# Kernel tuning notes

Measured on AMD Instinct MI355X. Metric: run time of the kernel, lower is better.

Reference implementation:

```python
import jax, jax.numpy as jnp
import numpy as np

N_NODES = 32767   # complete binary tree, depth 15
EMB_DIM = 256
HIDDEN = 256      # 'hidden_size' -> LSTM state is 2*HIDDEN
VOCAB = 32        # len(ExprNode.TYPE_LIST)


def setup_inputs() -> dict:
    key = jax.random.key(0)
    k1, k2, k3, k4, k5, k6 = jax.random.split(key, 6)
    H2 = 2 * HIDDEN
    types = jax.random.randint(k1, (N_NODES,), 0, VOCAB, dtype=jnp.int32)
    # complete binary tree: children of node i are 2i+1 / 2i+2; sentinel slot N = zero state
    idx = np.arange(N_NODES)
    a = 2 * idx + 1
    b = 2 * idx + 2
    a = np.where(a < N_NODES, a, N_NODES).astype(np.int32)
    b = np.where(b < N_NODES, b, N_NODES).astype(np.int32)
    scale = 1.0 / np.sqrt(H2)
    return {
        "types": types,
        "a_idx": jnp.asarray(a),
        "b_idx": jnp.asarray(b),
        "emb": jax.random.normal(k2, (VOCAB, EMB_DIM), jnp.float32) * 0.02,
        "W_ih": jax.random.normal(k3, (4 * H2, EMB_DIM), jnp.float32) * scale,
        "W_hh": jax.random.normal(k4, (4 * H2, H2), jnp.float32) * scale,
        "b_ih": jax.random.normal(k5, (4 * H2,), jnp.float32) * scale,
        "b_hh": jax.random.normal(k6, (4 * H2,), jnp.float32) * scale,
    }


def reference(types, a_idx, b_idx, emb, W_ih, W_hh, b_ih, b_hh):
    """Recursive binary tree-LSTM over topological (leaves-first) order.
    Each node's LSTM state has size 2H; a parent's incoming (h, c) is the concat
    of the first H entries of each child's state (zeros for missing children).
    Returns per-node hidden outputs [N, 2H] (the out_map, indexed by node id)."""
    N = types.shape[0]
    H2 = W_hh.shape[1]
    H = H2 // 2
    # batched input projection for all nodes at once: [N, 4*H2]
    x_proj = emb[types] @ W_ih.T + (b_ih + b_hh)
    Hs0 = jnp.zeros((N + 1, H2), x_proj.dtype)  # slot N = h0 (zeros)
    Cs0 = jnp.zeros((N + 1, H2), x_proj.dtype)
    order = jnp.arange(N - 1, -1, -1)  # children (higher index) before parents

    def step(carry, i):
        Hs, Cs = carry
        h = jnp.concatenate([Hs[a_idx[i], :H], Hs[b_idx[i], :H]])  # [2H]
        c = jnp.concatenate([Cs[a_idx[i], :H], Cs[b_idx[i], :H]])
        gates = x_proj[i] + W_hh @ h                 # [4*H2], torch gate order i,f,g,o
        ig, fg, gg, og = jnp.split(gates, 4)
        c_new = jax.nn.sigmoid(fg) * c + jax.nn.sigmoid(ig) * jnp.tanh(gg)
        h_new = jax.nn.sigmoid(og) * jnp.tanh(c_new)
        return (Hs.at[i].set(h_new), Cs.at[i].set(c_new)), h_new

    _, outs = jax.lax.scan(step, (Hs0, Cs0), order)
    return outs[::-1]  # reorder so row i is node i's output
```

## Files before the change

### kernel.cpp

```cpp
#include <hip/hip_runtime.h>
#include <hip/hip_bf16.h>


#define NNODES 32767

typedef __attribute__((ext_vector_type(8))) short bf16x8;
typedef __attribute__((ext_vector_type(4))) float f32x4;

__device__ __forceinline__ float sigf(float x) { return 1.0f / (1.0f + __expf(-x)); }
__device__ __forceinline__ float tanhfast(float x) { return 2.0f / (1.0f + __expf(-2.0f * x)) - 1.0f; }

__device__ __forceinline__ short bf_hi(float x) {
    __hip_bfloat16 h = __float2bfloat16(x);
    return __builtin_bit_cast(short, h);
}
__device__ __forceinline__ float bf_f(short s) {
    __hip_bfloat16 h = __builtin_bit_cast(__hip_bfloat16, s);
    return __bfloat162float(h);
}
__device__ __forceinline__ void split8(const float* src, short* hi, short* lo) {
#pragma unroll
    for (int j = 0; j < 8; ++j) {
        float x = src[j];
        short h = bf_hi(x);
        hi[j] = h;
        lo[j] = bf_hi(x - bf_f(h));
    }
}

__global__ void proj_kernel(const float* __restrict__ emb, const float* __restrict__ W_ih,
                            const float* __restrict__ b_ih, const float* __restrict__ b_hh,
                            float* __restrict__ proj) {
    __shared__ float e[256];
    int v = blockIdx.x >> 3;
    int rc = blockIdx.x & 7;
    int t = threadIdx.x;
    e[t] = emb[v * 256 + t];
    __syncthreads();
    int r = rc * 256 + t;
    const float4* w4 = (const float4*)(W_ih + (size_t)r * 256);
    const float4* e4 = (const float4*)e;
    float acc = 0.f;
#pragma unroll 8
    for (int k = 0; k < 64; ++k) {
        float4 w = w4[k];
        float4 h = e4[k];
        acc += w.x * h.x + w.y * h.y + w.z * h.z + w.w * h.w;
    }
    proj[v * 2048 + r] = acc + b_ih[r] + b_hh[r];
}

__global__ void wpack_kernel(const float* __restrict__ W_hh,
                             short* __restrict__ Whi, short* __restrict__ Wlo) {
    int t = blockIdx.x * 256 + threadIdx.x;
    int lane = t & 63;
    int kt = (t >> 6) & 15;
    int ntile = t >> 10;
    int n = ntile * 16 + (lane & 15);
    int k0 = kt * 32 + (lane >> 4) * 8;
    const float* src = W_hh + (size_t)n * 512 + k0;
    short hi[8], lo[8];
    split8(src, hi, lo);
    *(bf16x8*)(Whi + (size_t)t * 8) = *(bf16x8*)hi;
    *(bf16x8*)(Wlo + (size_t)t * 8) = *(bf16x8*)lo;
}

__global__ void leaf_kernel(const int* __restrict__ types, const float* __restrict__ proj,
                            float* __restrict__ out, float* __restrict__ C256,
                            short* __restrict__ Hsplit) {
    int bi = blockIdx.x;
    int node = 16383 + (bi >> 1);
    int j = ((bi & 1) << 8) + threadIdx.x;
    int tt = types[node];
    const float* p = proj + (size_t)tt * 2048;
    float gi = p[j];
    float gg = p[1024 + j];
    float go = p[1536 + j];
    float cn = sigf(gi) * tanhfast(gg);
    float hn = sigf(go) * tanhfast(cn);
    out[(size_t)node * 512 + j] = hn;
    if ((bi & 1) == 0) {
        C256[(size_t)node * 256 + j] = cn;
        short hi = bf_hi(hn);
        Hsplit[(size_t)node * 512 + j] = hi;
        Hsplit[(size_t)node * 512 + 256 + j] = bf_hi(hn - bf_f(hi));
    }
}

__global__ __launch_bounds__(512) void gemm_lstm_big(
    const int* __restrict__ a_idx, const int* __restrict__ b_idx,
    const int* __restrict__ types, float* __restrict__ out,
    const short* __restrict__ Whi, const short* __restrict__ Wlo,
    const float* __restrict__ proj, float* __restrict__ C256,
    short* __restrict__ Hsplit, int node_base, int Jc) {
    __shared__ short Ahi[4][16][64][8];
    __shared__ short Alo[4][16][64][8];
    __shared__ int sA[64], sB[64], sT[64];
    int t = threadIdx.x;
    int node0 = node_base + blockIdx.x * 64;
    if (t < 64) {
        sA[t] = a_idx[node0 + t];
        sB[t] = b_idx[node0 + t];
        sT[t] = types[node0 + t];
    }
    __syncthreads();

#pragma unroll
    for (int it = 0; it < 8; ++it) {
        int c = it * 512 + t;
        int mt = c >> 10;
        int kt = (c >> 6) & 15;
        int lane = c & 63;
        int m_loc = mt * 16 + (lane & 15);
        int k0 = kt * 32 + (lane >> 4) * 8;
        int child = (k0 < 256) ? sA[m_loc] : sB[m_loc];
        const short* src = Hsplit + (size_t)child * 512 + (k0 & 255);
        *(bf16x8*)&Ahi[mt][kt][lane][0] = *(const bf16x8*)src;
        *(bf16x8*)&Alo[mt][kt][lane][0] = *(const bf16x8*)(src + 256);
    }
    __syncthreads();

    int w = t >> 6;
    int lane = t & 63;
    int jsteps = Jc >> 4;
    int jbase = blockIdx.y * Jc;

    for (int js = w; js < jsteps; js += 8) {
        int j0 = jbase + js * 16;
        f32x4 acc[4][4];
#pragma unroll
        for (int q = 0; q < 4; ++q)
#pragma unroll
            for (int mt = 0; mt < 4; ++mt) acc[q][mt] = (f32x4){0.f, 0.f, 0.f, 0.f};
        int nt0 = j0 >> 4;

        for (int kt = 0; kt < 16; ++kt) {
            bf16x8 ah[4], al[4];
#pragma unroll
            for (int mt = 0; mt < 4; ++mt) {
                ah[mt] = *(const bf16x8*)&Ahi[mt][kt][lane][0];
                al[mt] = *(const bf16x8*)&Alo[mt][kt][lane][0];
            }
#pragma unroll
            for (int q = 0; q < 4; ++q) {
                int ntile = q * 32 + nt0;
                size_t off = ((size_t)(ntile * 16 + kt) * 64 + lane) * 8;
                bf16x8 bh = *(const bf16x8*)(Whi + off);
                bf16x8 bl = *(const bf16x8*)(Wlo + off);
#pragma unroll
                for (int mt = 0; mt < 4; ++mt) {
                    acc[q][mt] = __builtin_amdgcn_mfma_f32_16x16x32_bf16(ah[mt], bh, acc[q][mt], 0, 0, 0);
                    acc[q][mt] = __builtin_amdgcn_mfma_f32_16x16x32_bf16(ah[mt], bl, acc[q][mt], 0, 0, 0);
                    acc[q][mt] = __builtin_amdgcn_mfma_f32_16x16x32_bf16(al[mt], bh, acc[q][mt], 0, 0, 0);
                }
            }
        }

        int j = j0 + (lane & 15);
        int jc = j & 255;
        bool fh = (j < 256);
#pragma unroll
        for (int mt = 0; mt < 4; ++mt) {
            int mrow = mt * 16 + (lane >> 4) * 4;
#pragma unroll
            for (int r = 0; r < 4; ++r) {
                int m_loc = mrow + r;
                int node = node0 + m_loc;
                const float* p = proj + (size_t)sT[m_loc] * 2048 + j;
                float gi = acc[0][mt][r] + p[0];
                float gf = acc[1][mt][r] + p[512];
                float gg = acc[2][mt][r] + p[1024];
                float go = acc[3][mt][r] + p[1536];
                int child = fh ? sA[m_loc] : sB[m_loc];
                float c = C256[(size_t)child * 256 + jc];
                float cn = sigf(gf) * c + sigf(gi) * tanhfast(gg);
                float hn = sigf(go) * tanhfast(cn);
                out[(size_t)node * 512 + j] = hn;
                if (fh) {
                    C256[(size_t)node * 256 + j] = cn;
                    short hi = bf_hi(hn);
                    Hsplit[(size_t)node * 512 + j] = hi;
                    Hsplit[(size_t)node * 512 + 256 + j] = bf_hi(hn - bf_f(hi));
                }
            }
        }
    }
}

__global__ __launch_bounds__(256) void gemm_lstm_kernel(
    const int* __restrict__ a_idx, const int* __restrict__ b_idx,
    const int* __restrict__ types, float* __restrict__ out,
    const short* __restrict__ Whi, const short* __restrict__ Wlo,
    const float* __restrict__ proj, float* __restrict__ C256,
    short* __restrict__ Hsplit, int node_base, int Jc) {
    __shared__ short Ahi[2][16][64][8];
    __shared__ short Alo[2][16][64][8];
    __shared__ int sA[32], sB[32], sT[32];
    int t = threadIdx.x;
    int node0 = node_base + blockIdx.x * 32;
    if (t < 32) {
        sA[t] = a_idx[node0 + t];
        sB[t] = b_idx[node0 + t];
        sT[t] = types[node0 + t];
    }
    __syncthreads();

#pragma unroll
    for (int it = 0; it < 8; ++it) {
        int c = it * 256 + t;
        int mt = c >> 10;
        int kt = (c >> 6) & 15;
        int lane = c & 63;
        int m_loc = mt * 16 + (lane & 15);
        int k0 = kt * 32 + (lane >> 4) * 8;
        int child = (k0 < 256) ? sA[m_loc] : sB[m_loc];
        const short* src = Hsplit + (size_t)child * 512 + (k0 & 255);
        *(bf16x8*)&Ahi[mt][kt][lane][0] = *(const bf16x8*)src;
        *(bf16x8*)&Alo[mt][kt][lane][0] = *(const bf16x8*)(src + 256);
    }
    __syncthreads();

    int w = t >> 6;
    int lane = t & 63;
    int jsteps = Jc >> 4;
    int jbase = blockIdx.y * Jc;

    auto epilogue = [&](int j0, f32x4 (&acc)[4][2]) {
        int j = j0 + (lane & 15);
        int jc = j & 255;
        bool fh = (j < 256);
#pragma unroll
        for (int mt = 0; mt < 2; ++mt) {
            int mrow = mt * 16 + (lane >> 4) * 4;
#pragma unroll
            for (int r = 0; r < 4; ++r) {
                int m_loc = mrow + r;
                int node = node0 + m_loc;
                const float* p = proj + (size_t)sT[m_loc] * 2048 + j;
                float gi = acc[0][mt][r] + p[0];
                float gf = acc[1][mt][r] + p[512];
                float gg = acc[2][mt][r] + p[1024];
                float go = acc[3][mt][r] + p[1536];
                int child = fh ? sA[m_loc] : sB[m_loc];
                float c = C256[(size_t)child * 256 + jc];
                float cn = sigf(gf) * c + sigf(gi) * tanhfast(gg);
                float hn = sigf(go) * tanhfast(cn);
                out[(size_t)node * 512 + j] = hn;
                if (fh) {
                    C256[(size_t)node * 256 + j] = cn;
                    short hi = bf_hi(hn);
                    Hsplit[(size_t)node * 512 + j] = hi;
                    Hsplit[(size_t)node * 512 + 256 + j] = bf_hi(hn - bf_f(hi));
                }
            }
        }
    };

    if (jsteps >= 4) {
        for (int js = w; js < jsteps; js += 4) {
            int j0 = jbase + js * 16;
            f32x4 acc[4][2];
#pragma unroll
            for (int q = 0; q < 4; ++q)
#pragma unroll
                for (int mt = 0; mt < 2; ++mt) acc[q][mt] = (f32x4){0.f, 0.f, 0.f, 0.f};
            int nt0 = j0 >> 4;
            for (int kt = 0; kt < 16; ++kt) {
                bf16x8 ah0 = *(const bf16x8*)&Ahi[0][kt][lane][0];
                bf16x8 al0 = *(const bf16x8*)&Alo[0][kt][lane][0];
                bf16x8 ah1 = *(const bf16x8*)&Ahi[1][kt][lane][0];
                bf16x8 al1 = *(const bf16x8*)&Alo[1][kt][lane][0];
#pragma unroll
                for (int q = 0; q < 4; ++q) {
                    int ntile = q * 32 + nt0;
                    size_t off = ((size_t)(ntile * 16 + kt) * 64 + lane) * 8;
                    bf16x8 bh = *(const bf16x8*)(Whi + off);
                    bf16x8 bl = *(const bf16x8*)(Wlo + off);
                    acc[q][0] = __builtin_amdgcn_mfma_f32_16x16x32_bf16(ah0, bh, acc[q][0], 0, 0, 0);
                    acc[q][0] = __builtin_amdgcn_mfma_f32_16x16x32_bf16(ah0, bl, acc[q][0], 0, 0, 0);
                    acc[q][0] = __builtin_amdgcn_mfma_f32_16x16x32_bf16(al0, bh, acc[q][0], 0, 0, 0);
                    acc[q][1] = __builtin_amdgcn_mfma_f32_16x16x32_bf16(ah1, bh, acc[q][1], 0, 0, 0);
                    acc[q][1] = __builtin_amdgcn_mfma_f32_16x16x32_bf16(ah1, bl, acc[q][1], 0, 0, 0);
                    acc[q][1] = __builtin_amdgcn_mfma_f32_16x16x32_bf16(al1, bh, acc[q][1], 0, 0, 0);
                }
            }
            epilogue(j0, acc);
        }
    } else {
        int js = w & 1;
        int khalf = w >> 1;
        int j0 = jbase + js * 16;
        f32x4 acc[4][2];
#pragma unroll
        for (int q = 0; q < 4; ++q)
#pragma unroll
            for (int mt = 0; mt < 2; ++mt) acc[q][mt] = (f32x4){0.f, 0.f, 0.f, 0.f};
        int nt0 = j0 >> 4;
        int kt0 = khalf * 8;
        for (int kt = kt0; kt < kt0 + 8; ++kt) {
            bf16x8 ah0 = *(const bf16x8*)&Ahi[0][kt][lane][0];
            bf16x8 al0 = *(const bf16x8*)&Alo[0][kt][lane][0];
            bf16x8 ah1 = *(const bf16x8*)&Ahi[1][kt][lane][0];
            bf16x8 al1 = *(const bf16x8*)&Alo[1][kt][lane][0];
#pragma unroll
            for (int q = 0; q < 4; ++q) {
                int ntile = q * 32 + nt0;
                size_t off = ((size_t)(ntile * 16 + kt) * 64 + lane) * 8;
                bf16x8 bh = *(const bf16x8*)(Whi + off);
                bf16x8 bl = *(const bf16x8*)(Wlo + off);
                acc[q][0] = __builtin_amdgcn_mfma_f32_16x16x32_bf16(ah0, bh, acc[q][0], 0, 0, 0);
                acc[q][0] = __builtin_amdgcn_mfma_f32_16x16x32_bf16(ah0, bl, acc[q][0], 0, 0, 0);
                acc[q][0] = __builtin_amdgcn_mfma_f32_16x16x32_bf16(al0, bh, acc[q][0], 0, 0, 0);
                acc[q][1] = __builtin_amdgcn_mfma_f32_16x16x32_bf16(ah1, bh, acc[q][1], 0, 0, 0);
                acc[q][1] = __builtin_amdgcn_mfma_f32_16x16x32_bf16(ah1, bl, acc[q][1], 0, 0, 0);
                acc[q][1] = __builtin_amdgcn_mfma_f32_16x16x32_bf16(al1, bh, acc[q][1], 0, 0, 0);
            }
        }
        __syncthreads();
        float* xch = (float*)&Ahi[0][0][0][0];
        if (khalf == 1) {
#pragma unroll
            for (int q = 0; q < 4; ++q)
#pragma unroll
                for (int mt = 0; mt < 2; ++mt)
                    *(f32x4*)&xch[(((q * 2 + mt) * 128) + js * 64 + lane) * 4] = acc[q][mt];
        }
        __syncthreads();
        if (khalf == 0) {
#pragma unroll
            for (int q = 0; q < 4; ++q)
#pragma unroll
                for (int mt = 0; mt < 2; ++mt) {
                    f32x4 o = *(const f32x4*)&xch[(((q * 2 + mt) * 128) + js * 64 + lane) * 4];
                    acc[q][mt] += o;
                }
            epilogue(j0, acc);
        }
    }
}

__global__ void small_gemm_kernel(
    const int* __restrict__ a_idx, const int* __restrict__ b_idx,
    const float* __restrict__ out, const float* __restrict__ W_hh,
    float* __restrict__ part, int node_base) {
    __shared__ float hs[64];
    int t = threadIdx.x;
    int n = blockIdx.x;
    int node = node_base + n;
    int kbase = blockIdx.z * 64;
    if (t < 16) {
        int child = (kbase < 256) ? a_idx[node] : b_idx[node];
        float4 v = ((const float4*)(out + (size_t)child * 512 + (kbase & 255)))[t];
        ((float4*)hs)[t] = v;
    }
    __syncthreads();
    int r = blockIdx.y * 256 + t;
    const float4* w4 = (const float4*)(W_hh + (size_t)r * 512 + kbase);
    const float4* h4 = (const float4*)hs;
    float acc = 0.f;
#pragma unroll
    for (int k = 0; k < 16; ++k) {
        float4 wv = w4[k];
        float4 hv = h4[k];
        acc += wv.x * hv.x + wv.y * hv.y + wv.z * hv.z + wv.w * hv.w;
    }
    part[((size_t)blockIdx.z * gridDim.x + n) * 2048 + r] = acc;
}

__global__ void small_combine_kernel(
    const int* __restrict__ a_idx, const int* __restrict__ b_idx,
    const int* __restrict__ types, const float* __restrict__ part,
    const float* __restrict__ proj, float* __restrict__ C256,
    short* __restrict__ Hsplit, float* __restrict__ out, int node_base, int B) {
    int bi = blockIdx.x;
    int n = bi >> 1;
    int j = ((bi & 1) << 8) + threadIdx.x;
    int node = node_base + n;
    float g[4] = {0.f, 0.f, 0.f, 0.f};
    for (int z = 0; z < 8; ++z) {
        const float* p = part + ((size_t)z * B + n) * 2048;
#pragma unroll
        for (int q = 0; q < 4; ++q) g[q] += p[q * 512 + j];
    }
    const float* p = proj + (size_t)types[node] * 2048 + j;
    float gi = g[0] + p[0];
    float gf = g[1] + p[512];
    float gg = g[2] + p[1024];
    float go = g[3] + p[1536];
    int child = (j < 256) ? a_idx[node] : b_idx[node];
    float c = C256[(size_t)child * 256 + (j & 255)];
    float cn = sigf(gf) * c + sigf(gi) * tanhfast(gg);
    float hn = sigf(go) * tanhfast(cn);
    out[(size_t)node * 512 + j] = hn;
    if (j < 256) {
        C256[(size_t)node * 256 + j] = cn;
        short hi = bf_hi(hn);
        Hsplit[(size_t)node * 512 + j] = hi;
        Hsplit[(size_t)node * 512 + 256 + j] = bf_hi(hn - bf_f(hi));
    }
}

extern "C" void kernel_launch(void* const* d_in, const int* in_sizes, int n_in,
                              void* d_out, int out_size, void* d_ws, size_t ws_size,
                              hipStream_t stream) {
    const int* types = (const int*)d_in[0];
    const int* a_idx = (const int*)d_in[1];
    const int* b_idx = (const int*)d_in[2];
    const float* emb = (const float*)d_in[3];
    const float* W_ih = (const float*)d_in[4];
    const float* W_hh = (const float*)d_in[5];
    const float* b_ih = (const float*)d_in[6];
    const float* b_hh = (const float*)d_in[7];
    float* out = (float*)d_out;

    float* ws = (float*)d_ws;
    float* proj = ws;
    float* C256 = ws + 65536;
    short* Hsplit = (short*)(C256 + 8388352);
    short* Whi = Hsplit + 16777216;
    short* Wlo = Whi + 1048576;
    float* part = (float*)(Wlo + 1048576);

    proj_kernel<<<256, 256, 0, stream>>>(emb, W_ih, b_ih, b_hh, proj);
    wpack_kernel<<<512, 256, 0, stream>>>(W_hh, Whi, Wlo);
    leaf_kernel<<<32768, 256, 0, stream>>>(types, proj, out, C256, Hsplit);

    for (int d = 13; d >= 0; --d) {
        int base = (1 << d) - 1;
        int B = 1 << d;
        if (B >= 4096) {
            int J = (B == 8192) ? 2 : 4;
            gemm_lstm_big<<<dim3(B / 64, J), 512, 0, stream>>>(
                a_idx, b_idx, types, out, Whi, Wlo, proj, C256, Hsplit, base, 512 / J);
        } else if (B >= 32) {
            int bx = B / 32;
            int J = 2;
            while (bx * J < 512 && J < 16) J <<= 1;
            gemm_lstm_kernel<<<dim3(bx, J), 256, 0, stream>>>(
                a_idx, b_idx, types, out, Whi, Wlo, proj, C256, Hsplit, base, 512 / J);
        } else {
            small_gemm_kernel<<<dim3(B, 8, 8), 256, 0, stream>>>(
                a_idx, b_idx, out, W_hh, part, base);
            small_combine_kernel<<<B * 2, 256, 0, stream>>>(
                a_idx, b_idx, types, part, proj, C256, Hsplit, out, base, B);
        }
    }
}
```

Before: 477.4 us.

## Prefetch weight fragments, use nontemporal access, and linearize block order

```diff
diff --git a/kernel.cpp b/kernel.cpp
--- a/kernel.cpp
+++ b/kernel.cpp
@@ -78,12 +78,12 @@
     float go = p[1536 + j];
     float cn = sigf(gi) * tanhfast(gg);
     float hn = sigf(go) * tanhfast(cn);
-    out[(size_t)node * 512 + j] = hn;
+    __builtin_nontemporal_store(hn, &out[(size_t)node * 512 + j]);
     if ((bi & 1) == 0) {
-        C256[(size_t)node * 256 + j] = cn;
+        __builtin_nontemporal_store(cn, &C256[(size_t)node * 256 + j]);
         short hi = bf_hi(hn);
-        Hsplit[(size_t)node * 512 + j] = hi;
-        Hsplit[(size_t)node * 512 + 256 + j] = bf_hi(hn - bf_f(hi));
+        __builtin_nontemporal_store(hi, &Hsplit[(size_t)node * 512 + j]);
+        __builtin_nontemporal_store(bf_hi(hn - bf_f(hi)), &Hsplit[(size_t)node * 512 + 256 + j]);
     }
 }
 
@@ -92,12 +92,15 @@
     const int* __restrict__ types, float* __restrict__ out,
     const short* __restrict__ Whi, const short* __restrict__ Wlo,
     const float* __restrict__ proj, float* __restrict__ C256,
-    short* __restrict__ Hsplit, int node_base, int Jc) {
+    short* __restrict__ Hsplit, int node_base, int Jc, int jshift) {
     __shared__ short Ahi[4][16][64][8];
     __shared__ short Alo[4][16][64][8];
     __shared__ int sA[64], sB[64], sT[64];
     int t = threadIdx.x;
-    int node0 = node_base + blockIdx.x * 64;
+    int bid = blockIdx.x;
+    int by = bid & ((1 << jshift) - 1);
+    int bx = bid >> jshift;
+    int node0 = node_base + bx * 64;
     if (t < 64) {
         sA[t] = a_idx[node0 + t];
         sB[t] = b_idx[node0 + t];
@@ -114,27 +117,46 @@
         int m_loc = mt * 16 + (lane & 15);
         int k0 = kt * 32 + (lane >> 4) * 8;
         int child = (k0 < 256) ? sA[m_loc] : sB[m_loc];
-        const short* src = Hsplit + (size_t)child * 512 + (k0 & 255);
-        *(bf16x8*)&Ahi[mt][kt][lane][0] = *(const bf16x8*)src;
-        *(bf16x8*)&Alo[mt][kt][lane][0] = *(const bf16x8*)(src + 256);
+        const bf16x8* src = (const bf16x8*)(Hsplit + (size_t)child * 512 + (k0 & 255));
+        *(bf16x8*)&Ahi[mt][kt][lane][0] = __builtin_nontemporal_load(src);
+        *(bf16x8*)&Alo[mt][kt][lane][0] = __builtin_nontemporal_load((const bf16x8*)((const short*)src + 256));
     }
     __syncthreads();
 
     int w = t >> 6;
     int lane = t & 63;
     int jsteps = Jc >> 4;
-    int jbase = blockIdx.y * Jc;
+    int jbase = by * Jc;
 
     for (int js = w; js < jsteps; js += 8) {
         int j0 = jbase + js * 16;
+        int nt0 = j0 >> 4;
         f32x4 acc[4][4];
 #pragma unroll
         for (int q = 0; q < 4; ++q)
 #pragma unroll
             for (int mt = 0; mt < 4; ++mt) acc[q][mt] = (f32x4){0.f, 0.f, 0.f, 0.f};
-        int nt0 = j0 >> 4;
+
+        size_t base_q[4];
+#pragma unroll
+        for (int q = 0; q < 4; ++q)
+            base_q[q] = ((size_t)((q * 32 + nt0) * 16) * 64 + lane) * 8;
+
+        bf16x8 bh[4], bl[4];
+#pragma unroll
+        for (int q = 0; q < 4; ++q) {
+            bh[q] = *(const bf16x8*)(Whi + base_q[q]);
+            bl[q] = *(const bf16x8*)(Wlo + base_q[q]);
+        }
 
         for (int kt = 0; kt < 16; ++kt) {
+            int ktn = (kt + 1) & 15;
+            bf16x8 nbh[4], nbl[4];
+#pragma unroll
+            for (int q = 0; q < 4; ++q) {
+                nbh[q] = *(const bf16x8*)(Whi + base_q[q] + (size_t)ktn * 512);
+                nbl[q] = *(const bf16x8*)(Wlo + base_q[q] + (size_t)ktn * 512);
+            }
             bf16x8 ah[4], al[4];
 #pragma unroll
             for (int mt = 0; mt < 4; ++mt) {
@@ -143,17 +165,15 @@
             }
 #pragma unroll
             for (int q = 0; q < 4; ++q) {
-                int ntile = q * 32 + nt0;
-                size_t off = ((size_t)(ntile * 16 + kt) * 64 + lane) * 8;
-                bf16x8 bh = *(const bf16x8*)(Whi + off);
-                bf16x8 bl = *(const bf16x8*)(Wlo + off);
 #pragma unroll
                 for (int mt = 0; mt < 4; ++mt) {
-                    acc[q][mt] = __builtin_amdgcn_mfma_f32_16x16x32_bf16(ah[mt], bh, acc[q][mt], 0, 0, 0);
-                    acc[q][mt] = __builtin_amdgcn_mfma_f32_16x16x32_bf16(ah[mt], bl, acc[q][mt], 0, 0, 0);
-                    acc[q][mt] = __builtin_amdgcn_mfma_f32_16x16x32_bf16(al[mt], bh, acc[q][mt], 0, 0, 0);
-                }
-            }
+                    acc[q][mt] = __builtin_amdgcn_mfma_f32_16x16x32_bf16(ah[mt], bh[q], acc[q][mt], 0, 0, 0);
+                    acc[q][mt] = __builtin_amdgcn_mfma_f32_16x16x32_bf16(ah[mt], bl[q], acc[q][mt], 0, 0, 0);
+                    acc[q][mt] = __builtin_amdgcn_mfma_f32_16x16x32_bf16(al[mt], bh[q], acc[q][mt], 0, 0, 0);
+                }
+            }
+#pragma unroll
+            for (int q = 0; q < 4; ++q) { bh[q] = nbh[q]; bl[q] = nbl[q]; }
         }
 
         int j = j0 + (lane & 15);
@@ -172,15 +192,15 @@
                 float gg = acc[2][mt][r] + p[1024];
                 float go = acc[3][mt][r] + p[1536];
                 int child = fh ? sA[m_loc] : sB[m_loc];
-                float c = C256[(size_t)child * 256 + jc];
+                float c = __builtin_nontemporal_load(&C256[(size_t)child * 256 + jc]);
                 float cn = sigf(gf) * c + sigf(gi) * tanhfast(gg);
                 float hn = sigf(go) * tanhfast(cn);
-                out[(size_t)node * 512 + j] = hn;
+                __builtin_nontemporal_store(hn, &out[(size_t)node * 512 + j]);
                 if (fh) {
-                    C256[(size_t)node * 256 + j] = cn;
+                    __builtin_nontemporal_store(cn, &C256[(size_t)node * 256 + j]);
                     short hi = bf_hi(hn);
-                    Hsplit[(size_t)node * 512 + j] = hi;
-                    Hsplit[(size_t)node * 512 + 256 + j] = bf_hi(hn - bf_f(hi));
+                    __builtin_nontemporal_store(hi, &Hsplit[(size_t)node * 512 + j]);
+                    __builtin_nontemporal_store(bf_hi(hn - bf_f(hi)), &Hsplit[(size_t)node * 512 + 256 + j]);
                 }
             }
         }
@@ -192,12 +212,15 @@
     const int* __restrict__ types, float* __restrict__ out,
     const short* __restrict__ Whi, const short* __restrict__ Wlo,
     const float* __restrict__ proj, float* __restrict__ C256,
-    short* __restrict__ Hsplit, int node_base, int Jc) {
+    short* __restrict__ Hsplit, int node_base, int Jc, int jshift) {
     __shared__ short Ahi[2][16][64][8];
     __shared__ short Alo[2][16][64][8];
     __shared__ int sA[32], sB[32], sT[32];
     int t = threadIdx.x;
-    int node0 = node_base + blockIdx.x * 32;
+    int bid = blockIdx.x;
+    int by = bid & ((1 << jshift) - 1);
+    int bx = bid >> jshift;
+    int node0 = node_base + bx * 32;
     if (t < 32) {
         sA[t] = a_idx[node0 + t];
         sB[t] = b_idx[node0 + t];
@@ -214,16 +237,16 @@
         int m_loc = mt * 16 + (lane & 15);
         int k0 = kt * 32 + (lane >> 4) * 8;
         int child = (k0 < 256) ? sA[m_loc] : sB[m_loc];
-        const short* src = Hsplit + (size_t)child * 512 + (k0 & 255);
-        *(bf16x8*)&Ahi[mt][kt][lane][0] = *(const bf16x8*)src;
-        *(bf16x8*)&Alo[mt][kt][lane][0] = *(const bf16x8*)(src + 256);
+        const bf16x8* src = (const bf16x8*)(Hsplit + (size_t)child * 512 + (k0 & 255));
+        *(bf16x8*)&Ahi[mt][kt][lane][0] = __builtin_nontemporal_load(src);
+        *(bf16x8*)&Alo[mt][kt][lane][0] = __builtin_nontemporal_load((const bf16x8*)((const short*)src + 256));
     }
     __syncthreads();
 
     int w = t >> 6;
     int lane = t & 63;
     int jsteps = Jc >> 4;
-    int jbase = blockIdx.y * Jc;
+    int jbase = by * Jc;
 
     auto epilogue = [&](int j0, f32x4 (&acc)[4][2]) {
         int j = j0 + (lane & 15);
@@ -242,15 +265,15 @@
                 float gg = acc[2][mt][r] + p[1024];
                 float go = acc[3][mt][r] + p[1536];
                 int child = fh ? sA[m_loc] : sB[m_loc];
-                float c = C256[(size_t)child * 256 + jc];
+                float c = __builtin_nontemporal_load(&C256[(size_t)child * 256 + jc]);
                 float cn = sigf(gf) * c + sigf(gi) * tanhfast(gg);
                 float hn = sigf(go) * tanhfast(cn);
-                out[(size_t)node * 512 + j] = hn;
+                __builtin_nontemporal_store(hn, &out[(size_t)node * 512 + j]);
                 if (fh) {
-                    C256[(size_t)node * 256 + j] = cn;
+                    __builtin_nontemporal_store(cn, &C256[(size_t)node * 256 + j]);
                     short hi = bf_hi(hn);
-                    Hsplit[(size_t)node * 512 + j] = hi;
-                    Hsplit[(size_t)node * 512 + 256 + j] = bf_hi(hn - bf_f(hi));
+                    __builtin_nontemporal_store(hi, &Hsplit[(size_t)node * 512 + j]);
+                    __builtin_nontemporal_store(bf_hi(hn - bf_f(hi)), &Hsplit[(size_t)node * 512 + 256 + j]);
                 }
             }
         }
@@ -259,30 +282,48 @@
     if (jsteps >= 4) {
         for (int js = w; js < jsteps; js += 4) {
             int j0 = jbase + js * 16;
+            int nt0 = j0 >> 4;
             f32x4 acc[4][2];
 #pragma unroll
             for (int q = 0; q < 4; ++q)
 #pragma unroll
                 for (int mt = 0; mt < 2; ++mt) acc[q][mt] = (f32x4){0.f, 0.f, 0.f, 0.f};
-            int nt0 = j0 >> 4;
+
+            size_t base_q[4];
+#pragma unroll
+            for (int q = 0; q < 4; ++q)
+                base_q[q] = ((size_t)((q * 32 + nt0) * 16) * 64 + lane) * 8;
+
+            bf16x8 bh[4], bl[4];
+#pragma unroll
+            for (int q = 0; q < 4; ++q) {
+                bh[q] = *(const bf16x8*)(Whi + base_q[q]);
+                bl[q] = *(const bf16x8*)(Wlo + base_q[q]);
+            }
+
             for (int kt = 0; kt < 16; ++kt) {
+                int ktn = (kt + 1) & 15;
+                bf16x8 nbh[4], nbl[4];
+#pragma unroll
+                for (int q = 0; q < 4; ++q) {
+                    nbh[q] = *(const bf16x8*)(Whi + base_q[q] + (size_t)ktn * 512);
+                    nbl[q] = *(const bf16x8*)(Wlo + base_q[q] + (size_t)ktn * 512);
+                }
                 bf16x8 ah0 = *(const bf16x8*)&Ahi[0][kt][lane][0];
                 bf16x8 al0 = *(const bf16x8*)&Alo[0][kt][lane][0];
                 bf16x8 ah1 = *(const bf16x8*)&Ahi[1][kt][lane][0];
                 bf16x8 al1 = *(const bf16x8*)&Alo[1][kt][lane][0];
 #pragma unroll
                 for (int q = 0; q < 4; ++q) {
-                    int ntile = q * 32 + nt0;
-                    size_t off = ((size_t)(ntile * 16 + kt) * 64 + lane) * 8;
-                    bf16x8 bh = *(const bf16x8*)(Whi + off);
-                    bf16x8 bl = *(const bf16x8*)(Wlo + off);
-                    acc[q][0] = __builtin_amdgcn_mfma_f32_16x16x32_bf16(ah0, bh, acc[q][0], 0, 0, 0);
-                    acc[q][0] = __builtin_amdgcn_mfma_f32_16x16x32_bf16(ah0, bl, acc[q][0], 0, 0, 0);
-                    acc[q][0] = __builtin_amdgcn_mfma_f32_16x16x32_bf16(al0, bh, acc[q][0], 0, 0, 0);
-                    acc[q][1] = __builtin_amdgcn_mfma_f32_16x16x32_bf16(ah1, bh, acc[q][1], 0, 0, 0);
-                    acc[q][1] = __builtin_amdgcn_mfma_f32_16x16x32_bf16(ah1, bl, acc[q][1], 0, 0, 0);
-                    acc[q][1] = __builtin_amdgcn_mfma_f32_16x16x32_bf16(al1, bh, acc[q][1], 0, 0, 0);
-                }
+                    acc[q][0] = __builtin_amdgcn_mfma_f32_16x16x32_bf16(ah0, bh[q], acc[q][0], 0, 0, 0);
+                    acc[q][0] = __builtin_amdgcn_mfma_f32_16x16x32_bf16(ah0, bl[q], acc[q][0], 0, 0, 0);
+                    acc[q][0] = __builtin_amdgcn_mfma_f32_16x16x32_bf16(al0, bh[q], acc[q][0], 0, 0, 0);
+                    acc[q][1] = __builtin_amdgcn_mfma_f32_16x16x32_bf16(ah1, bh[q], acc[q][1], 0, 0, 0);
+                    acc[q][1] = __builtin_amdgcn_mfma_f32_16x16x32_bf16(ah1, bl[q], acc[q][1], 0, 0, 0);
+                    acc[q][1] = __builtin_amdgcn_mfma_f32_16x16x32_bf16(al1, bh[q], acc[q][1], 0, 0, 0);
+                }
+#pragma unroll
+                for (int q = 0; q < 4; ++q) { bh[q] = nbh[q]; bl[q] = nbl[q]; }
             }
             epilogue(j0, acc);
         }
@@ -430,14 +471,15 @@
         int B = 1 << d;
         if (B >= 4096) {
             int J = (B == 8192) ? 2 : 4;
-            gemm_lstm_big<<<dim3(B / 64, J), 512, 0, stream>>>(
-                a_idx, b_idx, types, out, Whi, Wlo, proj, C256, Hsplit, base, 512 / J);
+            int jshift = (B == 8192) ? 1 : 2;
+            gemm_lstm_big<<<(B / 64) * J, 512, 0, stream>>>(
+                a_idx, b_idx, types, out, Whi, Wlo, proj, C256, Hsplit, base, 512 / J, jshift);
         } else if (B >= 32) {
             int bx = B / 32;
-            int J = 2;
-            while (bx * J < 512 && J < 16) J <<= 1;
-            gemm_lstm_kernel<<<dim3(bx, J), 256, 0, stream>>>(
-                a_idx, b_idx, types, out, Whi, Wlo, proj, C256, Hsplit, base, 512 / J);
+            int J = 2, jshift = 1;
+            while (bx * J < 512 && J < 16) { J <<= 1; ++jshift; }
+            gemm_lstm_kernel<<<bx * J, 256, 0, stream>>>(
+                a_idx, b_idx, types, out, Whi, Wlo, proj, C256, Hsplit, base, 512 / J, jshift);
         } else {
             small_gemm_kernel<<<dim3(B, 8, 8), 256, 0, stream>>>(
                 a_idx, b_idx, out, W_hh, part, base);
```

After: 483.8 us. No clear change (+1.3%).
